# Kernel tuning notes

Measured on AMD Instinct MI355X. Metric: run time of the kernel, lower is better.

## Reference

```python
import jax, jax.numpy as jnp
import numpy as np

B, H, N, D, M = 1, 4, 2048, 64, 256  # batch, heads, seq, dim_heads, nb_features
EPS = 1e-4


def _gaussian_orthogonal_random_matrix(nb_rows, nb_cols, seed=0):
    # scaling=1 path of the torch code: stacked transposed-Q orthogonal blocks,
    # scaled by sqrt(nb_cols).
    rng = np.random.default_rng(seed)
    blocks = []
    for _ in range(nb_rows // nb_cols):
        q, _ = np.linalg.qr(rng.standard_normal((nb_cols, nb_cols)))
        blocks.append(q.T)
    final = np.concatenate(blocks, axis=0)  # [nb_rows, nb_cols]
    return jnp.asarray(np.sqrt(float(nb_cols)) * final, dtype=jnp.float32)


def setup_inputs() -> dict:
    key = jax.random.key(0)
    kq, kk, kv = jax.random.split(key, 3)
    return {
        "q": jax.random.normal(kq, (B, H, N, D), dtype=jnp.float32),
        "k": jax.random.normal(kk, (B, H, N, D), dtype=jnp.float32),
        "v": jax.random.normal(kv, (B, H, N, D), dtype=jnp.float32),
        "projection_matrix": _gaussian_orthogonal_random_matrix(M, D),
    }


def _softmax_kernel(data, projection_matrix, is_query):
    # data: [B,H,N,D], projection_matrix: [M,D] -> features [B,H,N,M]
    data_normalizer = 1.0 / data.shape[-1] ** 0.25
    ratio = 1.0 / projection_matrix.shape[0] ** 0.5
    data_dash = jnp.einsum("bhnd,md->bhnm", data_normalizer * data, projection_matrix)
    diag_data = jnp.sum(data * data, axis=-1) * 0.5 * data_normalizer ** 2  # [B,H,N]
    diag_data = diag_data[..., None]  # [B,H,N,1]
    if is_query:
        stab = jnp.max(data_dash, axis=-1, keepdims=True)
    else:
        stab = jnp.max(data_dash)
    return ratio * (jnp.exp(data_dash - diag_data - stab) + EPS)


def _causal_linear_attention(q, k, v):
    # q,k: [B,H,N,M] features; v: [B,H,N,E]
    k_cumsum = jnp.cumsum(k, axis=-2)                       # [B,H,N,M]
    context = jnp.einsum("bhnm,bhne->bhnme", k, v)          # outer products
    context = jnp.cumsum(context, axis=-3)                  # cumulative over n
    context = context / k_cumsum[..., None]                 # [B,H,N,M,E]
    return jnp.einsum("bhnme,bhnm->bhne", context, q)


def reference(q, k, v, projection_matrix):
    q_feat = _softmax_kernel(q, projection_matrix, is_query=True)
    k_feat = _softmax_kernel(k, projection_matrix, is_query=False)
    return _causal_linear_attention(q_feat, k_feat, v)
```

## Files before the change

kernel.cpp:

```cpp
#include <hip/hip_runtime.h>
#include <math.h>

#define NH   4
#define SEQ  2048
#define DH   64
#define NF   256
#define ROWS (NH*SEQ)
#define DN    0.35355339059327373f
#define DIAGC 0.0625f
#define RATIO 0.0625f
#define EPSF  1e-4f

typedef __attribute__((ext_vector_type(8))) short bf8;
typedef __attribute__((ext_vector_type(4))) short bf4;
typedef __attribute__((ext_vector_type(4))) float f4;

static __device__ __forceinline__ unsigned short f2bf(float x) {
  union { float f; unsigned u; } v; v.f = x;
  unsigned r = v.u + 0x7FFF + ((v.u >> 16) & 1);
  return (unsigned short)(r >> 16);
}
static __device__ __forceinline__ float bf2f(unsigned short b) {
  union { unsigned u; float f; } v; v.u = ((unsigned)b) << 16;
  return v.f;
}

__global__ __launch_bounds__(256) void k_proj(const float* __restrict__ q,
    const float* __restrict__ k, const float* __restrict__ v,
    const float* __restrict__ P,
    unsigned short* __restrict__ qfb, float* __restrict__ dshd,
    float* __restrict__ bmax, unsigned short* __restrict__ vtb) {
  __shared__ float lds[64*65];
  const int b = blockIdx.x;
  if (b >= 1024) {
    const int cb = b - 1024;
    const int h = cb >> 5, n0 = (cb & 31) * 64;
    const int tid = threadIdx.x;
    for (int i = tid; i < 4096; i += 256) {
      int n = i >> 6, e = i & 63;
      lds[n*65 + e] = v[((size_t)h*SEQ + n0 + n)*DH + e];
    }
    __syncthreads();
    for (int i = tid; i < 4096; i += 256) {
      int e = i >> 6, n = i & 63;
      vtb[((size_t)h*DH + e)*SEQ + n0 + n] = f2bf(lds[n*65 + e]);
    }
    return;
  }
  const bool isq = b < 512;
  const int tile = isq ? b : b - 512;
  const int w = threadIdx.x >> 6, lane = threadIdx.x & 63;
  const int lr = lane & 15, g = lane >> 4;
  const float* x = (isq ? q : k) + (size_t)tile*16*DH;

  f4 a  = *(const f4*)(x + lr*DH + g*8);
  f4 bb = *(const f4*)(x + lr*DH + g*8 + 4);
  f4 c  = *(const f4*)(x + lr*DH + 32 + g*8);
  f4 d  = *(const f4*)(x + lr*DH + 32 + g*8 + 4);
  float ss = 0.f;
#pragma unroll
  for (int i = 0; i < 4; ++i) ss += a[i]*a[i] + bb[i]*bb[i] + c[i]*c[i] + d[i]*d[i];
  ss += __shfl_xor(ss, 16);
  ss += __shfl_xor(ss, 32);

  bf8 xh0, xh1, xl0, xl1;
#pragma unroll
  for (int i = 0; i < 4; ++i) {
    float v0 = DN*a[i], v1 = DN*bb[i], v2 = DN*c[i], v3 = DN*d[i];
    unsigned short h0 = f2bf(v0), h1 = f2bf(v1), h2 = f2bf(v2), h3 = f2bf(v3);
    xh0[i] = (short)h0; xh0[i+4] = (short)h1;
    xh1[i] = (short)h2; xh1[i+4] = (short)h3;
    xl0[i]   = (short)f2bf(v0 - bf2f(h0)); xl0[i+4] = (short)f2bf(v1 - bf2f(h1));
    xl1[i]   = (short)f2bf(v2 - bf2f(h2)); xl1[i+4] = (short)f2bf(v3 - bf2f(h3));
  }

  const int ct0 = w*4;
  f4 dsh[4];
#pragma unroll
  for (int cc = 0; cc < 4; ++cc) {
    const int ct = ct0 + cc;
    const float* prow = P + (ct*16 + lr)*DH + g*8;
    f4 p0 = *(const f4*)(prow);
    f4 p1 = *(const f4*)(prow + 4);
    f4 p2 = *(const f4*)(prow + 32);
    f4 p3 = *(const f4*)(prow + 36);
    bf8 bh0, bl0, bh1, bl1;
#pragma unroll
    for (int i = 0; i < 4; ++i) {
      unsigned short h0 = f2bf(p0[i]), h1 = f2bf(p1[i]);
      unsigned short h2 = f2bf(p2[i]), h3 = f2bf(p3[i]);
      bh0[i] = (short)h0; bh0[i+4] = (short)h1;
      bh1[i] = (short)h2; bh1[i+4] = (short)h3;
      bl0[i]   = (short)f2bf(p0[i] - bf2f(h0)); bl0[i+4] = (short)f2bf(p1[i] - bf2f(h1));
      bl1[i]   = (short)f2bf(p2[i] - bf2f(h2)); bl1[i+4] = (short)f2bf(p3[i] - bf2f(h3));
    }
    f4 acc = {0.f, 0.f, 0.f, 0.f};
    acc = __builtin_amdgcn_mfma_f32_16x16x32_bf16(xh0, bh0, acc, 0, 0, 0);
    acc = __builtin_amdgcn_mfma_f32_16x16x32_bf16(xh1, bh1, acc, 0, 0, 0);
    acc = __builtin_amdgcn_mfma_f32_16x16x32_bf16(xh0, bl0, acc, 0, 0, 0);
    acc = __builtin_amdgcn_mfma_f32_16x16x32_bf16(xh1, bl1, acc, 0, 0, 0);
    acc = __builtin_amdgcn_mfma_f32_16x16x32_bf16(xl0, bh0, acc, 0, 0, 0);
    acc = __builtin_amdgcn_mfma_f32_16x16x32_bf16(xl1, bh1, acc, 0, 0, 0);
    dsh[cc] = acc;
  }

  f4 mr;
#pragma unroll
  for (int r = 0; r < 4; ++r)
    mr[r] = fmaxf(fmaxf(dsh[0][r], dsh[1][r]), fmaxf(dsh[2][r], dsh[3][r]));
#pragma unroll
  for (int mk = 1; mk <= 8; mk <<= 1) {
#pragma unroll
    for (int r = 0; r < 4; ++r) mr[r] = fmaxf(mr[r], __shfl_xor(mr[r], mk));
  }
  if (lr == 0) {
#pragma unroll
    for (int r = 0; r < 4; ++r) lds[w*16 + 4*g + r] = mr[r];
  }
  __syncthreads();
  float rm[4], sr[4];
#pragma unroll
  for (int r = 0; r < 4; ++r) {
    rm[r] = fmaxf(fmaxf(lds[0*16 + 4*g + r], lds[1*16 + 4*g + r]),
                  fmaxf(lds[2*16 + 4*g + r], lds[3*16 + 4*g + r]));
    sr[r] = __shfl(ss, 4*g + r);
  }

  if (isq) {
    unsigned short* ob = qfb + (size_t)tile*16*NF;
#pragma unroll
    for (int cc = 0; cc < 4; ++cc) {
#pragma unroll
      for (int r = 0; r < 4; ++r)
        ob[(4*g + r)*NF + (ct0 + cc)*16 + lr] =
            f2bf(RATIO*(expf(dsh[cc][r] - (sr[r]*DIAGC + rm[r])) + EPSF));
    }
  } else {
    float* db = dshd + (size_t)tile*16*NF;
#pragma unroll
    for (int cc = 0; cc < 4; ++cc) {
#pragma unroll
      for (int r = 0; r < 4; ++r)
        db[(4*g + r)*NF + (ct0 + cc)*16 + lr] = dsh[cc][r] - sr[r]*DIAGC;
    }
    if (w == 0 && lr == 0) {
#pragma unroll
      for (int r = 0; r < 4; ++r) bmax[tile*16 + 4*g + r] = mr[r];
    }
  }
}

__global__ __launch_bounds__(256) void k_feat2(const float* __restrict__ dshd,
    const float* __restrict__ bmax, unsigned short* __restrict__ kfb,
    unsigned short* __restrict__ kft, float* __restrict__ csum) {
  const int u = blockIdx.x, m = threadIdx.x;
  const int h = u >> 7, t = u & 127;
  __shared__ float red[256];
  float mx = -3.4e38f;
  for (int i = m; i < ROWS; i += 256) mx = fmaxf(mx, bmax[i]);
  red[m] = mx;
  __syncthreads();
  for (int s = 128; s > 0; s >>= 1) {
    if (m < s) red[m] = fmaxf(red[m], red[m+s]);
    __syncthreads();
  }
  const float gg = red[0];
  const float* db = dshd + (size_t)u*16*NF + m;
  unsigned short* ob = kfb + (size_t)u*16*NF + m;
  float run = 0.f;
  bf8 k0, k1;
#pragma unroll
  for (int r = 0; r < 16; ++r) {
    unsigned short bv = f2bf(RATIO*(expf(db[r*NF] - gg) + EPSF));
    ob[r*NF] = bv;
    if (r < 8) k0[r] = (short)bv; else k1[r-8] = (short)bv;
    run += bf2f(bv);
  }
  csum[(size_t)u*NF + m] = run;
  unsigned short* kt = kft + ((size_t)(h*NF + m))*SEQ + t*16;
  *(bf8*)kt = k0;
  *(bf8*)(kt + 8) = k1;
}

__global__ __launch_bounds__(64) void k_state(
    const unsigned short* __restrict__ vtb, const unsigned short* __restrict__ kft,
    unsigned short* __restrict__ sthi, unsigned short* __restrict__ stlo,
    float* __restrict__ csum) {
  const int bx = blockIdx.x;
  if (bx >= 256) {
    const int h = bx - 256;
    const int m0 = threadIdx.x * 4;
    f4 run = {0.f, 0.f, 0.f, 0.f};
#pragma unroll 4
    for (int c = 0; c < 128; ++c) {
      float* p = csum + ((size_t)(h*128 + c))*NF + m0;
      f4 x = *(const f4*)p;
      *(f4*)p = run;
      run += x;
    }
    return;
  }
  const int lane = threadIdx.x;
  const int lr = lane & 15, g = lane >> 4;
  const int h = bx >> 6, et = (bx >> 4) & 3, mt = bx & 15;

  const unsigned short* vb = vtb + ((size_t)(h*DH + et*16 + lr))*SEQ;
  const unsigned short* kb = kft + ((size_t)(h*NF + mt*16 + lr))*SEQ;

  f4 cum = {0.f, 0.f, 0.f, 0.f};
  for (int c = 0; c < 16; ++c) {
    const size_t base = ((size_t)((h*16 + c)*64 + et*16 + 4*g))*NF + mt*16 + lr;
#pragma unroll
    for (int r = 0; r < 4; ++r) {
      unsigned short hi = f2bf(cum[r]);
      sthi[base + (size_t)r*NF] = hi;
      stlo[base + (size_t)r*NF] = f2bf(cum[r] - bf2f(hi));
    }
#pragma unroll
    for (int ks = 0; ks < 4; ++ks) {
      const int j0 = c*128 + ks*32 + g*8;
      bf8 xv = *(const bf8*)(vb + j0);
      bf8 ym = *(const bf8*)(kb + j0);
      cum = __builtin_amdgcn_mfma_f32_16x16x32_bf16(xv, ym, cum, 0, 0, 0);
    }
  }
}

__global__ __launch_bounds__(128) void k_attn3(const unsigned short* __restrict__ qpb,
                                               const unsigned short* __restrict__ kfb,
                                               const unsigned short* __restrict__ vtb,
                                               const unsigned short* __restrict__ sthi,
                                               const unsigned short* __restrict__ stlo,
                                               const float* __restrict__ csum,
                                               float* __restrict__ out) {
  const int h = blockIdx.y;
  const int b = blockIdx.x;
  const int c = b >> 2, qt = b & 3;
  const int tid = threadIdx.x;
  const int wid = tid >> 6, lane = tid & 63;
  const int t = c*8 + qt*2 + wid;
  const int lr = lane & 15, g = lane >> 4;
  const int jc0 = c*8;
  const int nstage = qt*2 + 2;

  __shared__ __align__(16) char smem[26624];
  char* Ks = smem + 16384;
  char* Vs = smem + 24576;

  {
    const int u = h*128 + t;
    f4 run = *(const f4*)(csum + (size_t)u*NF + lane*4);
    const unsigned short* kfp = kfb + ((size_t)(h*SEQ + t*16))*NF + lane*4;
    const unsigned short* qfp = qpb + ((size_t)(h*SEQ + t*16))*NF + lane*4;
#pragma unroll
    for (int r = 0; r < 16; ++r) {
      bf4 kv = *(const bf4*)(kfp + (size_t)r*NF);
      bf4 qv = *(const bf4*)(qfp + (size_t)r*NF);
      unsigned short qp[4];
#pragma unroll
      for (int i = 0; i < 4; ++i) {
        run[i] += bf2f((unsigned short)kv[i]);
        qp[i] = f2bf(bf2f((unsigned short)qv[i]) / run[i]);
      }
      const int rloc = wid*16 + r;
      const int byte = (rloc*512 + lane*8) ^ ((rloc & 7) << 4);
      *(bf4*)(smem + byte) = *(bf4*)qp;
    }
  }
  __syncthreads();

  bf8 qf[8];
  {
    const int rloc = wid*16 + lr;
#pragma unroll
    for (int kb = 0; kb < 8; ++kb) {
      const int byte = (rloc*512 + g*16 + kb*64) ^ ((rloc & 7) << 4);
      qf[kb] = *(const bf8*)(smem + byte);
    }
  }

  const char* kTile = (const char*)(kfb + (size_t)h*SEQ*NF);
  const char* vTile = (const char*)(vtb + (size_t)h*DH*SEQ);

  const int ko0 = wid*4096 +    0 + lane*16;
  const int ko1 = wid*4096 + 1024 + lane*16;
  const int ko2 = wid*4096 + 2048 + lane*16;
  const int ko3 = wid*4096 + 3072 + lane*16;
  const int kw0 = ko0 ^ (((ko0 >> 9) & 7) << 4);
  const int kw1 = ko1 ^ (((ko1 >> 9) & 7) << 4);
  const int kw2 = ko2 ^ (((ko2 >> 9) & 7) << 4);
  const int kw3 = ko3 ^ (((ko3 >> 9) & 7) << 4);
  const int vo = tid*16;
  const int ve = vo >> 5;
  const int vn = vo & 31;

  f4 sk0, sk1, sk2, sk3, sv;
  {
    const char* kt = kTile + (size_t)jc0*8192;
    sk0 = *(const f4*)(kt + ko0);
    sk1 = *(const f4*)(kt + ko1);
    sk2 = *(const f4*)(kt + ko2);
    sk3 = *(const f4*)(kt + ko3);
    sv  = *(const f4*)(vTile + (size_t)ve*4096 + (size_t)jc0*32 + vn);
  }

  f4 o0 = {0,0,0,0}, o1 = {0,0,0,0}, o2 = {0,0,0,0}, o3 = {0,0,0,0};
  {
    const unsigned short* SH = sthi + ((size_t)((h*16 + c)*64 + lr))*NF + g*8;
    const unsigned short* SL = stlo + ((size_t)((h*16 + c)*64 + lr))*NF + g*8;
#pragma unroll
    for (int ks = 0; ks < 8; ++ks) {
#pragma unroll
      for (int et = 0; et < 4; ++et) {
        bf8 bh = *(const bf8*)(SH + et*16*NF + ks*32);
        bf8 bl = *(const bf8*)(SL + et*16*NF + ks*32);
        f4 acc = (et == 0) ? o0 : (et == 1) ? o1 : (et == 2) ? o2 : o3;
        acc = __builtin_amdgcn_mfma_f32_16x16x32_bf16(qf[ks], bh, acc, 0, 0, 0);
        acc = __builtin_amdgcn_mfma_f32_16x16x32_bf16(qf[ks], bl, acc, 0, 0, 0);
        if (et == 0) o0 = acc; else if (et == 1) o1 = acc; else if (et == 2) o2 = acc; else o3 = acc;
      }
    }
  }

  for (int jj = 0; jj < nstage; ++jj) {
    const int j = jc0 + jj;
    *(f4*)(Ks + kw0) = sk0;
    *(f4*)(Ks + kw1) = sk1;
    *(f4*)(Ks + kw2) = sk2;
    *(f4*)(Ks + kw3) = sk3;
    *(f4*)(Vs + vo) = sv;
    __syncthreads();
    if (jj + 1 < nstage) {
      const char* kt = kTile + (size_t)(j+1)*8192;
      sk0 = *(const f4*)(kt + ko0);
      sk1 = *(const f4*)(kt + ko1);
      sk2 = *(const f4*)(kt + ko2);
      sk3 = *(const f4*)(kt + ko3);
      sv  = *(const f4*)(vTile + (size_t)ve*4096 + (size_t)(j+1)*32 + vn);
    }
    if (j <= t) {
      bf8 kcs[8];
#pragma unroll
      for (int kb = 0; kb < 8; ++kb) {
        int off = (lr*512 + kb*64 + g*16) ^ ((lr & 7) << 4);
        kcs[kb] = *(const bf8*)(Ks + off);
      }
      f4 st = {0,0,0,0};
#pragma unroll
      for (int kb = 0; kb < 8; ++kb)
        st = __builtin_amdgcn_mfma_f32_16x16x32_bf16(kcs[kb], qf[kb], st, 0, 0, 0);
      if (j == t) {
#pragma unroll
        for (int rr = 0; rr < 4; ++rr) if (g*4 + rr > lr) st[rr] = 0.f;
      }
      bf8 sb = { (short)f2bf(st[0]), (short)f2bf(st[1]), (short)f2bf(st[2]), (short)f2bf(st[3]),
                 (short)0, (short)0, (short)0, (short)0 };
#pragma unroll
      for (int eb = 0; eb < 4; ++eb) {
        bf4 v4 = *(const bf4*)(Vs + (eb*16 + lr)*32 + g*8);
        bf8 vf = { v4[0], v4[1], v4[2], v4[3], (short)0, (short)0, (short)0, (short)0 };
        f4 acc = (eb == 0) ? o0 : (eb == 1) ? o1 : (eb == 2) ? o2 : o3;
        acc = __builtin_amdgcn_mfma_f32_16x16x32_bf16(sb, vf, acc, 0, 0, 0);
        if (eb == 0) o0 = acc; else if (eb == 1) o1 = acc; else if (eb == 2) o2 = acc; else o3 = acc;
      }
    }
    __syncthreads();
  }

  float* ob = out + ((size_t)(h*SEQ + t*16))*DH;
#pragma unroll
  for (int rr = 0; rr < 4; ++rr) {
    ob[(size_t)(4*g + rr)*DH +  0 + lr] = o0[rr];
    ob[(size_t)(4*g + rr)*DH + 16 + lr] = o1[rr];
    ob[(size_t)(4*g + rr)*DH + 32 + lr] = o2[rr];
    ob[(size_t)(4*g + rr)*DH + 48 + lr] = o3[rr];
  }
}

extern "C" void kernel_launch(void* const* d_in, const int* in_sizes, int n_in,
                              void* d_out, int out_size, void* d_ws, size_t ws_size,
                              hipStream_t stream) {
  const float* q = (const float*)d_in[0];
  const float* k = (const float*)d_in[1];
  const float* v = (const float*)d_in[2];
  const float* P = (const float*)d_in[3];
  float* out = (float*)d_out;

  char* ws = (char*)d_ws;
  unsigned short* qfb  = (unsigned short*)(ws);
  unsigned short* kfb  = (unsigned short*)(ws + (4u<<20));
  unsigned short* vtb  = (unsigned short*)(ws + (8u<<20));
  unsigned short* kft  = (unsigned short*)(ws + (12u<<20));
  float* dshd   = (float*)(ws + (16u<<20));
  float* bmax   = (float*)(ws + (24u<<20));
  float* csum   = (float*)(ws + (25u<<20));
  unsigned short* sthi = (unsigned short*)(ws + (33u<<20));
  unsigned short* stlo = (unsigned short*)(ws + (36u<<20));

  k_proj  <<<1152, 256, 0, stream>>>(q, k, v, P, qfb, dshd, bmax, vtb);
  k_feat2 <<<512, 256, 0, stream>>>(dshd, bmax, kfb, kft, csum);
  k_state <<<260, 64, 0, stream>>>(vtb, kft, sthi, stlo, csum);
  k_attn3 <<<dim3(64, NH), 128, 0, stream>>>(qfb, kfb, vtb, sthi, stlo, csum, out);
}
```

Measured before the change: 57.88 us.

## Split state scan across two waves, one-wave attention blocks, per-tile key max

The key-projection kernel now reduces the row max to one value per 16-row tile with wave shuffles. This shrinks the global-max read in k_feat2 from 8192 entries to 512. k_state now runs two waves per block, each scanning half of the chunks; a shared-memory bridge then adds the first half's total into the second half's prefix states, halving the serial MFMA chain. The attention kernel moves to one 64-thread wave per query tile with 512 blocks, which removes all __syncthreads and the stages that were skipped on the causal diagonal, at the cost of each wave loading full K/V tiles alone.

```diff
diff --git a/kernel.cpp b/kernel.cpp
--- a/kernel.cpp
+++ b/kernel.cpp
@@ -143,10 +143,10 @@
       for (int r = 0; r < 4; ++r)
         db[(4*g + r)*NF + (ct0 + cc)*16 + lr] = dsh[cc][r] - sr[r]*DIAGC;
     }
-    if (w == 0 && lr == 0) {
-#pragma unroll
-      for (int r = 0; r < 4; ++r) bmax[tile*16 + 4*g + r] = mr[r];
-    }
+    float tmax = fmaxf(fmaxf(rm[0], rm[1]), fmaxf(rm[2], rm[3]));
+    tmax = fmaxf(tmax, __shfl_xor(tmax, 16));
+    tmax = fmaxf(tmax, __shfl_xor(tmax, 32));
+    if (w == 0 && lane == 0) bmax[tile] = tmax;
   }
 }
 
@@ -156,9 +156,7 @@
   const int u = blockIdx.x, m = threadIdx.x;
   const int h = u >> 7, t = u & 127;
   __shared__ float red[256];
-  float mx = -3.4e38f;
-  for (int i = m; i < ROWS; i += 256) mx = fmaxf(mx, bmax[i]);
-  red[m] = mx;
+  red[m] = fmaxf(bmax[m], bmax[m + 256]);
   __syncthreads();
   for (int s = 128; s > 0; s >>= 1) {
     if (m < s) red[m] = fmaxf(red[m], red[m+s]);
@@ -182,12 +180,13 @@
   *(bf8*)(kt + 8) = k1;
 }
 
-__global__ __launch_bounds__(64) void k_state(
+__global__ __launch_bounds__(128) void k_state(
     const unsigned short* __restrict__ vtb, const unsigned short* __restrict__ kft,
     unsigned short* __restrict__ sthi, unsigned short* __restrict__ stlo,
     float* __restrict__ csum) {
   const int bx = blockIdx.x;
   if (bx >= 256) {
+    if (threadIdx.x >= 64) return;
     const int h = bx - 256;
     const int m0 = threadIdx.x * 4;
     f4 run = {0.f, 0.f, 0.f, 0.f};
@@ -200,7 +199,8 @@
     }
     return;
   }
-  const int lane = threadIdx.x;
+  __shared__ f4 bridge[64];
+  const int wid = threadIdx.x >> 6, lane = threadIdx.x & 63;
   const int lr = lane & 15, g = lane >> 4;
   const int h = bx >> 6, et = (bx >> 4) & 3, mt = bx & 15;
 
@@ -208,13 +208,21 @@
   const unsigned short* kb = kft + ((size_t)(h*NF + mt*16 + lr))*SEQ;
 
   f4 cum = {0.f, 0.f, 0.f, 0.f};
-  for (int c = 0; c < 16; ++c) {
-    const size_t base = ((size_t)((h*16 + c)*64 + et*16 + 4*g))*NF + mt*16 + lr;
-#pragma unroll
-    for (int r = 0; r < 4; ++r) {
-      unsigned short hi = f2bf(cum[r]);
-      sthi[base + (size_t)r*NF] = hi;
-      stlo[base + (size_t)r*NF] = f2bf(cum[r] - bf2f(hi));
+  f4 loc[8];
+  const int c0 = wid*8;
+#pragma unroll
+  for (int cc = 0; cc < 8; ++cc) {
+    const int c = c0 + cc;
+    if (wid == 0) {
+      const size_t base = ((size_t)((h*16 + c)*64 + et*16 + 4*g))*NF + mt*16 + lr;
+#pragma unroll
+      for (int r = 0; r < 4; ++r) {
+        unsigned short hi = f2bf(cum[r]);
+        sthi[base + (size_t)r*NF] = hi;
+        stlo[base + (size_t)r*NF] = f2bf(cum[r] - bf2f(hi));
+      }
+    } else {
+      loc[cc] = cum;
     }
 #pragma unroll
     for (int ks = 0; ks < 4; ++ks) {
@@ -224,28 +232,43 @@
       cum = __builtin_amdgcn_mfma_f32_16x16x32_bf16(xv, ym, cum, 0, 0, 0);
     }
   }
-}
-
-__global__ __launch_bounds__(128) void k_attn3(const unsigned short* __restrict__ qpb,
-                                               const unsigned short* __restrict__ kfb,
-                                               const unsigned short* __restrict__ vtb,
-                                               const unsigned short* __restrict__ sthi,
-                                               const unsigned short* __restrict__ stlo,
-                                               const float* __restrict__ csum,
-                                               float* __restrict__ out) {
+  if (wid == 0) bridge[lane] = cum;
+  __syncthreads();
+  if (wid == 1) {
+    f4 s8 = bridge[lane];
+#pragma unroll
+    for (int cc = 0; cc < 8; ++cc) {
+      const int c = 8 + cc;
+      f4 val = s8 + loc[cc];
+      const size_t base = ((size_t)((h*16 + c)*64 + et*16 + 4*g))*NF + mt*16 + lr;
+#pragma unroll
+      for (int r = 0; r < 4; ++r) {
+        unsigned short hi = f2bf(val[r]);
+        sthi[base + (size_t)r*NF] = hi;
+        stlo[base + (size_t)r*NF] = f2bf(val[r] - bf2f(hi));
+      }
+    }
+  }
+}
+
+__global__ __launch_bounds__(64) void k_attn4(const unsigned short* __restrict__ qpb,
+                                              const unsigned short* __restrict__ kfb,
+                                              const unsigned short* __restrict__ vtb,
+                                              const unsigned short* __restrict__ sthi,
+                                              const unsigned short* __restrict__ stlo,
+                                              const float* __restrict__ csum,
+                                              float* __restrict__ out) {
   const int h = blockIdx.y;
-  const int b = blockIdx.x;
-  const int c = b >> 2, qt = b & 3;
-  const int tid = threadIdx.x;
-  const int wid = tid >> 6, lane = tid & 63;
-  const int t = c*8 + qt*2 + wid;
+  const int t = blockIdx.x;
+  const int c = t >> 3;
+  const int jc0 = c*8;
+  const int nstage = (t & 7) + 1;
+  const int lane = threadIdx.x;
   const int lr = lane & 15, g = lane >> 4;
-  const int jc0 = c*8;
-  const int nstage = qt*2 + 2;
-
-  __shared__ __align__(16) char smem[26624];
-  char* Ks = smem + 16384;
-  char* Vs = smem + 24576;
+
+  __shared__ __align__(16) char smem[18432];
+  char* Ks = smem + 8192;
+  char* Vs = smem + 16384;
 
   {
     const int u = h*128 + t;
@@ -262,46 +285,36 @@
         run[i] += bf2f((unsigned short)kv[i]);
         qp[i] = f2bf(bf2f((unsigned short)qv[i]) / run[i]);
       }
-      const int rloc = wid*16 + r;
-      const int byte = (rloc*512 + lane*8) ^ ((rloc & 7) << 4);
+      const int byte = (r*512 + lane*8) ^ ((r & 7) << 4);
       *(bf4*)(smem + byte) = *(bf4*)qp;
     }
   }
-  __syncthreads();
 
   bf8 qf[8];
-  {
-    const int rloc = wid*16 + lr;
-#pragma unroll
-    for (int kb = 0; kb < 8; ++kb) {
-      const int byte = (rloc*512 + g*16 + kb*64) ^ ((rloc & 7) << 4);
-      qf[kb] = *(const bf8*)(smem + byte);
-    }
+#pragma unroll
+  for (int kb = 0; kb < 8; ++kb) {
+    const int byte = (lr*512 + g*16 + kb*64) ^ ((lr & 7) << 4);
+    qf[kb] = *(const bf8*)(smem + byte);
   }
 
   const char* kTile = (const char*)(kfb + (size_t)h*SEQ*NF);
   const char* vTile = (const char*)(vtb + (size_t)h*DH*SEQ);
 
-  const int ko0 = wid*4096 +    0 + lane*16;
-  const int ko1 = wid*4096 + 1024 + lane*16;
-  const int ko2 = wid*4096 + 2048 + lane*16;
-  const int ko3 = wid*4096 + 3072 + lane*16;
-  const int kw0 = ko0 ^ (((ko0 >> 9) & 7) << 4);
-  const int kw1 = ko1 ^ (((ko1 >> 9) & 7) << 4);
-  const int kw2 = ko2 ^ (((ko2 >> 9) & 7) << 4);
-  const int kw3 = ko3 ^ (((ko3 >> 9) & 7) << 4);
-  const int vo = tid*16;
-  const int ve = vo >> 5;
-  const int vn = vo & 31;
-
-  f4 sk0, sk1, sk2, sk3, sv;
+  int kw[8];
+#pragma unroll
+  for (int i = 0; i < 8; ++i) {
+    const int ko = i*1024 + lane*16;
+    kw[i] = ko ^ (((ko >> 9) & 7) << 4);
+  }
+
+  f4 sk[8], sv0, sv1;
   {
     const char* kt = kTile + (size_t)jc0*8192;
-    sk0 = *(const f4*)(kt + ko0);
-    sk1 = *(const f4*)(kt + ko1);
-    sk2 = *(const f4*)(kt + ko2);
-    sk3 = *(const f4*)(kt + ko3);
-    sv  = *(const f4*)(vTile + (size_t)ve*4096 + (size_t)jc0*32 + vn);
+#pragma unroll
+    for (int i = 0; i < 8; ++i) sk[i] = *(const f4*)(kt + i*1024 + lane*16);
+    const char* vt = vTile + (size_t)lane*4096 + (size_t)jc0*32;
+    sv0 = *(const f4*)(vt);
+    sv1 = *(const f4*)(vt + 16);
   }
 
   f4 o0 = {0,0,0,0}, o1 = {0,0,0,0}, o2 = {0,0,0,0}, o3 = {0,0,0,0};
@@ -324,47 +337,42 @@
 
   for (int jj = 0; jj < nstage; ++jj) {
     const int j = jc0 + jj;
-    *(f4*)(Ks + kw0) = sk0;
-    *(f4*)(Ks + kw1) = sk1;
-    *(f4*)(Ks + kw2) = sk2;
-    *(f4*)(Ks + kw3) = sk3;
-    *(f4*)(Vs + vo) = sv;
-    __syncthreads();
+#pragma unroll
+    for (int i = 0; i < 8; ++i) *(f4*)(Ks + kw[i]) = sk[i];
+    *(f4*)(Vs + lane*32) = sv0;
+    *(f4*)(Vs + lane*32 + 16) = sv1;
     if (jj + 1 < nstage) {
       const char* kt = kTile + (size_t)(j+1)*8192;
-      sk0 = *(const f4*)(kt + ko0);
-      sk1 = *(const f4*)(kt + ko1);
-      sk2 = *(const f4*)(kt + ko2);
-      sk3 = *(const f4*)(kt + ko3);
-      sv  = *(const f4*)(vTile + (size_t)ve*4096 + (size_t)(j+1)*32 + vn);
-    }
-    if (j <= t) {
-      bf8 kcs[8];
-#pragma unroll
-      for (int kb = 0; kb < 8; ++kb) {
-        int off = (lr*512 + kb*64 + g*16) ^ ((lr & 7) << 4);
-        kcs[kb] = *(const bf8*)(Ks + off);
-      }
-      f4 st = {0,0,0,0};
-#pragma unroll
-      for (int kb = 0; kb < 8; ++kb)
-        st = __builtin_amdgcn_mfma_f32_16x16x32_bf16(kcs[kb], qf[kb], st, 0, 0, 0);
-      if (j == t) {
-#pragma unroll
-        for (int rr = 0; rr < 4; ++rr) if (g*4 + rr > lr) st[rr] = 0.f;
-      }
-      bf8 sb = { (short)f2bf(st[0]), (short)f2bf(st[1]), (short)f2bf(st[2]), (short)f2bf(st[3]),
-                 (short)0, (short)0, (short)0, (short)0 };
-#pragma unroll
-      for (int eb = 0; eb < 4; ++eb) {
-        bf4 v4 = *(const bf4*)(Vs + (eb*16 + lr)*32 + g*8);
-        bf8 vf = { v4[0], v4[1], v4[2], v4[3], (short)0, (short)0, (short)0, (short)0 };
-        f4 acc = (eb == 0) ? o0 : (eb == 1) ? o1 : (eb == 2) ? o2 : o3;
-        acc = __builtin_amdgcn_mfma_f32_16x16x32_bf16(sb, vf, acc, 0, 0, 0);
-        if (eb == 0) o0 = acc; else if (eb == 1) o1 = acc; else if (eb == 2) o2 = acc; else o3 = acc;
-      }
-    }
-    __syncthreads();
+#pragma unroll
+      for (int i = 0; i < 8; ++i) sk[i] = *(const f4*)(kt + i*1024 + lane*16);
+      const char* vt = vTile + (size_t)lane*4096 + (size_t)(j+1)*32;
+      sv0 = *(const f4*)(vt);
+      sv1 = *(const f4*)(vt + 16);
+    }
+    bf8 kcs[8];
+#pragma unroll
+    for (int kb = 0; kb < 8; ++kb) {
+      int off = (lr*512 + kb*64 + g*16) ^ ((lr & 7) << 4);
+      kcs[kb] = *(const bf8*)(Ks + off);
+    }
+    f4 st = {0,0,0,0};
+#pragma unroll
+    for (int kb = 0; kb < 8; ++kb)
+      st = __builtin_amdgcn_mfma_f32_16x16x32_bf16(kcs[kb], qf[kb], st, 0, 0, 0);
+    if (j == t) {
+#pragma unroll
+      for (int rr = 0; rr < 4; ++rr) if (g*4 + rr > lr) st[rr] = 0.f;
+    }
+    bf8 sb = { (short)f2bf(st[0]), (short)f2bf(st[1]), (short)f2bf(st[2]), (short)f2bf(st[3]),
+               (short)0, (short)0, (short)0, (short)0 };
+#pragma unroll
+    for (int eb = 0; eb < 4; ++eb) {
+      bf4 v4 = *(const bf4*)(Vs + (eb*16 + lr)*32 + g*8);
+      bf8 vf = { v4[0], v4[1], v4[2], v4[3], (short)0, (short)0, (short)0, (short)0 };
+      f4 acc = (eb == 0) ? o0 : (eb == 1) ? o1 : (eb == 2) ? o2 : o3;
+      acc = __builtin_amdgcn_mfma_f32_16x16x32_bf16(sb, vf, acc, 0, 0, 0);
+      if (eb == 0) o0 = acc; else if (eb == 1) o1 = acc; else if (eb == 2) o2 = acc; else o3 = acc;
+    }
   }
 
   float* ob = out + ((size_t)(h*SEQ + t*16))*DH;
@@ -399,6 +407,6 @@
 
   k_proj  <<<1152, 256, 0, stream>>>(q, k, v, P, qfb, dshd, bmax, vtb);
   k_feat2 <<<512, 256, 0, stream>>>(dshd, bmax, kfb, kft, csum);
-  k_state <<<260, 64, 0, stream>>>(vtb, kft, sthi, stlo, csum);
-  k_attn3 <<<dim3(64, NH), 128, 0, stream>>>(qfb, kfb, vtb, sthi, stlo, csum, out);
-}
+  k_state <<<260, 128, 0, stream>>>(vtb, kft, sthi, stlo, csum);
+  k_attn4 <<<dim3(128, NH), 64, 0, stream>>>(qfb, kfb, vtb, sthi, stlo, csum, out);
+}
```

Result: faster. 54.34 us (-6.1%).
